# Performance work log

Measured on AMD Instinct MI355X. Metric: run time of the kernel, lower is better.

Reference implementation:

```python
import jax, jax.numpy as jnp
import numpy as np

B, T, IN, H, OUT = 32, 1024, 256, 768, 128


def setup_inputs() -> dict:
    key = jax.random.key(0)
    ks = jax.random.split(key, 11)
    s = 0.05
    return {
        "x": jax.random.normal(ks[0], (B, T, IN), dtype=jnp.float32),
        "W_ih0": jax.random.normal(ks[1], (4 * H, IN), dtype=jnp.float32) * s,
        "W_hh0": jax.random.normal(ks[2], (4 * H, H), dtype=jnp.float32) * s,
        "b_ih0": jax.random.normal(ks[3], (4 * H,), dtype=jnp.float32) * s,
        "b_hh0": jax.random.normal(ks[4], (4 * H,), dtype=jnp.float32) * s,
        "W_ih1": jax.random.normal(ks[5], (4 * H, H), dtype=jnp.float32) * s,
        "W_hh1": jax.random.normal(ks[6], (4 * H, H), dtype=jnp.float32) * s,
        "b_ih1": jax.random.normal(ks[7], (4 * H,), dtype=jnp.float32) * s,
        "b_hh1": jax.random.normal(ks[8], (4 * H,), dtype=jnp.float32) * s,
        "W_lin": jax.random.normal(ks[9], (OUT, H), dtype=jnp.float32) * s,
        "b_lin": jax.random.normal(ks[10], (OUT,), dtype=jnp.float32) * s,
    }


def _lstm_layer(x_btd, W_ih, W_hh, b_ih, b_hh):
    # Input-side GEMM for all timesteps at once: [B,T,4H]
    xg = jnp.einsum("btd,gd->btg", x_btd, W_ih) + b_ih + b_hh
    xg = jnp.swapaxes(xg, 0, 1)  # time-major [T,B,4H]
    h0 = jnp.zeros((x_btd.shape[0], W_hh.shape[1]), x_btd.dtype)

    def step(carry, gx):
        h, c = carry
        g = gx + h @ W_hh.T  # [B,4H]
        i, f, gg, o = jnp.split(g, 4, axis=-1)  # PyTorch gate order i,f,g,o
        i, f, o = jax.nn.sigmoid(i), jax.nn.sigmoid(f), jax.nn.sigmoid(o)
        c = f * c + i * jnp.tanh(gg)
        h = o * jnp.tanh(c)
        return (h, c), h

    _, hs = jax.lax.scan(step, (h0, h0), xg)  # hs: [T,B,H]
    return jnp.swapaxes(hs, 0, 1)  # [B,T,H]


def reference(x, W_ih0, W_hh0, b_ih0, b_hh0, W_ih1, W_hh1, b_ih1, b_hh1, W_lin, b_lin):
    h1 = _lstm_layer(x, W_ih0, W_hh0, b_ih0, b_hh0)
    h2 = _lstm_layer(h1, W_ih1, W_hh1, b_ih1, b_hh1)  # eval mode: inter-layer dropout off
    return jnp.einsum("bth,oh->bto", h2, W_lin) + b_lin
```

## Files before the change

### kernel.cpp

```cpp
#include <hip/hip_runtime.h>

#define Tt    1024
#define INF   256
#define Hh    768
#define OUTF  128

#define NWG_L0  48
#define NWG_L1  48
#define NWG_LIN 2
#define NWG     (NWG_L0 + NWG_L1 + NWG_LIN)
#define NTHR    1024

typedef unsigned int       u32;
typedef unsigned long long u64;
typedef unsigned short     u16;
typedef __attribute__((ext_vector_type(8))) short bf16x8;
typedef __attribute__((ext_vector_type(4))) float f32x4;

#define PROG_OFF 0
#define HA_OFF   16384
#define HB_OFF   (HA_OFF + 3*49152)
#define WS_BYTES (HB_OFF + 3*49152)
#define HPS      24576

#define ASTR_B 1552
#define RSLAB  272
#define RROW   17

__device__ __forceinline__ float sigf(float v){ return 1.0f/(1.0f+__expf(-v)); }
__device__ __forceinline__ float tanhfast(float x){
    const float cx = fminf(fmaxf(x, -15.f), 15.f);
    const float e  = __expf(2.f * cx);
    return (e - 1.f) / (e + 1.f);
}
__device__ __forceinline__ u16 f2bf(float f){
    u32 u = __float_as_uint(f);
    return (u16)((u + 0x7fffu + ((u>>16)&1u)) >> 16);
}
__device__ __forceinline__ void st32ws(u16* p, u32 v){
    __hip_atomic_store((u32*)p, v, __ATOMIC_RELAXED, __HIP_MEMORY_SCOPE_AGENT);
}
__device__ __forceinline__ u32 ldu32(const u32* p){
    return __hip_atomic_load(p, __ATOMIC_RELAXED, __HIP_MEMORY_SCOPE_AGENT);
}
__device__ __forceinline__ void stu32(u32* p, u32 v){
    __hip_atomic_store(p, v, __ATOMIC_RELAXED, __HIP_MEMORY_SCOPE_AGENT);
}
__device__ __forceinline__ void ld16x3(const u16* p0, const u16* p1, const u16* p2,
                                       f32x4& r0, f32x4& r1, f32x4& r2){
    asm volatile(
        "global_load_dwordx4 %0, %3, off sc0 sc1\n\t"
        "global_load_dwordx4 %1, %4, off sc0 sc1\n\t"
        "global_load_dwordx4 %2, %5, off sc0 sc1\n\t"
        "s_waitcnt vmcnt(0)"
        : "=&v"(r0), "=&v"(r1), "=&v"(r2)
        : "v"(p0), "v"(p1), "v"(p2)
        : "memory");
}
__device__ __forceinline__ void ld16x6(const u16* p0, const u16* p1, const u16* p2,
                                       const u16* p3, const u16* p4, const u16* p5,
                                       f32x4& r0, f32x4& r1, f32x4& r2,
                                       f32x4& r3, f32x4& r4, f32x4& r5){
    asm volatile(
        "global_load_dwordx4 %0, %6, off sc0 sc1\n\t"
        "global_load_dwordx4 %1, %7, off sc0 sc1\n\t"
        "global_load_dwordx4 %2, %8, off sc0 sc1\n\t"
        "global_load_dwordx4 %3, %9, off sc0 sc1\n\t"
        "global_load_dwordx4 %4, %10, off sc0 sc1\n\t"
        "global_load_dwordx4 %5, %11, off sc0 sc1\n\t"
        "s_waitcnt vmcnt(0)"
        : "=&v"(r0), "=&v"(r1), "=&v"(r2), "=&v"(r3), "=&v"(r4), "=&v"(r5)
        : "v"(p0), "v"(p1), "v"(p2), "v"(p3), "v"(p4), "v"(p5)
        : "memory");
}

__device__ __forceinline__ void waitlines(u32* prog, int base, int cnt, u32 thr, int lane){
    bool ok = (lane >= cnt);
    int guard = 0;
    while (guard < (1 << 24)) {
        if (!ok) ok = (ldu32(prog + (base + lane) * 32) >= thr);
        if (__ballot(ok) == ~0ull) break;
        __builtin_amdgcn_s_sleep(1);
        ++guard;
    }
}

__global__ void prologue(char* ws){
    int i = blockIdx.x * 256 + threadIdx.x;
    if (i < WS_BYTES / 4)
        __hip_atomic_store(((u32*)ws) + i, 0u, __ATOMIC_RELAXED, __HIP_MEMORY_SCOPE_AGENT);
}

__device__ __forceinline__ bf16x8 load8w(const float* p){
    float4 v0 = *(const float4*)(p);
    float4 v1 = *(const float4*)(p + 4);
    bf16x8 r;
    r[0]=(short)f2bf(v0.x); r[1]=(short)f2bf(v0.y); r[2]=(short)f2bf(v0.z); r[3]=(short)f2bf(v0.w);
    r[4]=(short)f2bf(v1.x); r[5]=(short)f2bf(v1.y); r[6]=(short)f2bf(v1.z); r[7]=(short)f2bf(v1.w);
    return r;
}

__global__ __launch_bounds__(NTHR) void lstm_persist(
    const float* __restrict__ x,
    const float* __restrict__ Wih0, const float* __restrict__ Whh0,
    const float* __restrict__ bih0, const float* __restrict__ bhh0,
    const float* __restrict__ Wih1, const float* __restrict__ Whh1,
    const float* __restrict__ bih1, const float* __restrict__ bhh1,
    const float* __restrict__ Wlin, const float* __restrict__ blin,
    float* __restrict__ out, char* ws)
{
    u32* prog = (u32*)(ws + PROG_OFF);
    u16* hA   = (u16*)(ws + HA_OFF);
    u16* hB   = (u16*)(ws + HB_OFF);

    const int wg  = blockIdx.x;
    const int tid = threadIdx.x;

    __shared__ __align__(16) char smem[49664];
    char*  actb = smem;
    float* red  = (float*)smem;

    const int lane = tid & 63, w = tid >> 6;
    const int quad = lane >> 4, nl = lane & 15;
    const int nt = w >> 2, ks = w & 3;
    const int b3 = tid >> 5, q = tid & 31;

    const int role  = (wg < NWG_L0) ? 0 : ((wg < NWG_L0 + NWG_L1) ? 1 : 2);
    const int jbase = (role == 0) ? wg * 16 : ((role == 1) ? (wg - NWG_L0) * 16 : 0);
    const int obase = (role == 2) ? (wg - NWG_L0 - NWG_L1) * 64 : 0;

    bf16x8 bfr[12];
    if (role == 0) {
        const int grow = nt * Hh + jbase + nl;
        #pragma unroll
        for (int fi = 0; fi < 8; ++fi) {
            const int c = fi >> 2, fc = fi & 3;
            const int ka = c * 512 + ks * 128 + fc * 32 + quad * 8;
            const float* p = (ka < 256) ? (Wih0 + (size_t)grow * 256 + ka)
                                        : (Whh0 + (size_t)grow * 768 + (ka - 256));
            bfr[fi] = load8w(p);
        }
    } else if (role == 1) {
        const int grow = nt * Hh + jbase + nl;
        #pragma unroll
        for (int fi = 0; fi < 12; ++fi) {
            const int c = fi / 6, fc = fi % 6;
            const int ka = c * 768 + ks * 192 + fc * 32 + quad * 8;
            const float* p = (ka < 768) ? (Wih1 + (size_t)grow * 768 + ka)
                                        : (Whh1 + (size_t)grow * 768 + (ka - 768));
            bfr[fi] = load8w(p);
        }
    } else {
        const int row = obase + nt * 16 + nl;
        #pragma unroll
        for (int fi = 0; fi < 6; ++fi) {
            const int ka = ks * 192 + fi * 32 + quad * 8;
            bfr[fi] = load8w(Wlin + (size_t)row * 768 + ka);
        }
    }

    float ba0=0,ba1=0,ba2=0,ba3=0, bb0=0,bb1=0,bb2=0,bb3=0, creg0=0, creg1=0;
    float bl0 = 0.f, bl1 = 0.f;
    if (role < 2 && tid < 256) {
        const int jg0 = jbase + 2 * (tid >> 5), jg1 = jg0 + 1;
        const float* bi = (role == 0) ? bih0 : bih1;
        const float* bh = (role == 0) ? bhh0 : bhh1;
        ba0 = bi[jg0]        + bh[jg0];        bb0 = bi[jg1]        + bh[jg1];
        ba1 = bi[768 + jg0]  + bh[768 + jg0];  bb1 = bi[768 + jg1]  + bh[768 + jg1];
        ba2 = bi[1536 + jg0] + bh[1536 + jg0]; bb2 = bi[1536 + jg1] + bh[1536 + jg1];
        ba3 = bi[2304 + jg0] + bh[2304 + jg0]; bb3 = bi[2304 + jg1] + bh[2304 + jg1];
    }
    if (role == 2) {
        bl0 = blin[obase + (tid >> 5)];
        bl1 = blin[obase + 32 + (tid >> 5)];
    }

    for (int s = 0; s < Tt + 2; ++s) {
        const bool active = (role == 0) ? (s < Tt)
                          : (role == 1) ? (s >= 1 && s <= Tt)
                          :               (s >= 2);
        const int par_wA = s % 3;
        const int par_rA = (s + 2) % 3;
        const int par_wB = (s + 2) % 3;
        const int par_rB = (s + 1) % 3;

        if (active && w == 0) {
            if (role == 0) {
                if (s >= 1) waitlines(prog, 0, 48, (u32)s, lane);
                if (s >= 2) waitlines(prog, 48, 48, (u32)(s - 1), lane);
            } else if (role == 1) {
                waitlines(prog, 48, 48, (u32)s, lane);
                {
                    const u32 thr2 = (lane < 48) ? (u32)s : (u32)(s - 1);
                    const int idx  = (lane < 48) ? lane : (96 + (lane - 48));
                    bool ok = (lane >= 50);
                    int guard = 0;
                    while (guard < (1 << 24)) {
                        if (!ok) ok = (ldu32(prog + idx * 32) >= thr2);
                        if (__ballot(ok) == ~0ull) break;
                        __builtin_amdgcn_s_sleep(1);
                        ++guard;
                    }
                }
            } else {
                waitlines(prog, 48, 48, (u32)s, lane);
            }
        }
        __syncthreads();

        if (active) {
            f32x4 acc0 = {0.f,0.f,0.f,0.f}, acc1 = {0.f,0.f,0.f,0.f};

            if (role == 0) {
                const float* xs = x + ((size_t)b3 * Tt + s) * INF + q * 8;
                const float4 v0 = *(const float4*)xs;
                const float4 v1 = *(const float4*)(xs + 4);
                const u16* hp = hA + (size_t)par_rA * HPS + b3 * 768;
                f32x4 h0, h1, h2;
                ld16x3(hp + q * 8, hp + 256 + q * 8, hp + 512 + q * 8, h0, h1, h2);
                {
                    uint4 xv;
                    xv.x = (u32)f2bf(v0.x) | ((u32)f2bf(v0.y) << 16);
                    xv.y = (u32)f2bf(v0.z) | ((u32)f2bf(v0.w) << 16);
                    xv.z = (u32)f2bf(v1.x) | ((u32)f2bf(v1.y) << 16);
                    xv.w = (u32)f2bf(v1.z) | ((u32)f2bf(v1.w) << 16);
                    *(uint4*)(actb + b3 * ASTR_B + q * 16) = xv;
                    *(f32x4*)(actb + b3 * ASTR_B + 512 + q * 16) = h0;
                }
                __syncthreads();
                #pragma unroll
                for (int fc = 0; fc < 4; ++fc) {
                    const int koff = ks * 128 + fc * 32 + quad * 8;
                    bf16x8 a0 = *(const bf16x8*)(actb + nl * ASTR_B + koff * 2);
                    bf16x8 a1 = *(const bf16x8*)(actb + (16 + nl) * ASTR_B + koff * 2);
                    acc0 = __builtin_amdgcn_mfma_f32_16x16x32_bf16(a0, bfr[fc], acc0, 0, 0, 0);
                    acc1 = __builtin_amdgcn_mfma_f32_16x16x32_bf16(a1, bfr[fc], acc1, 0, 0, 0);
                }
                __syncthreads();
                *(f32x4*)(actb + b3 * ASTR_B + q * 16)       = h1;
                *(f32x4*)(actb + b3 * ASTR_B + 512 + q * 16) = h2;
                __syncthreads();
                #pragma unroll
                for (int fc = 0; fc < 4; ++fc) {
                    const int koff = ks * 128 + fc * 32 + quad * 8;
                    bf16x8 a0 = *(const bf16x8*)(actb + nl * ASTR_B + koff * 2);
                    bf16x8 a1 = *(const bf16x8*)(actb + (16 + nl) * ASTR_B + koff * 2);
                    acc0 = __builtin_amdgcn_mfma_f32_16x16x32_bf16(a0, bfr[4 + fc], acc0, 0, 0, 0);
                    acc1 = __builtin_amdgcn_mfma_f32_16x16x32_bf16(a1, bfr[4 + fc], acc1, 0, 0, 0);
                }
                __syncthreads();
            } else if (role == 1) {
                const u16* pA = hA + (size_t)par_rA * HPS + b3 * 768;
                const u16* pB = hB + (size_t)par_rB * HPS + b3 * 768;
                f32x4 a0, a1, a2, bq0, bq1, bq2;
                ld16x6(pA + q * 8, pA + 256 + q * 8, pA + 512 + q * 8,
                       pB + q * 8, pB + 256 + q * 8, pB + 512 + q * 8,
                       a0, a1, a2, bq0, bq1, bq2);
                *(f32x4*)(actb + b3 * ASTR_B + q * 16)        = a0;
                *(f32x4*)(actb + b3 * ASTR_B + 512 + q * 16)  = a1;
                *(f32x4*)(actb + b3 * ASTR_B + 1024 + q * 16) = a2;
                __syncthreads();
                #pragma unroll
                for (int fc = 0; fc < 6; ++fc) {
                    const int koff = ks * 192 + fc * 32 + quad * 8;
                    bf16x8 f0 = *(const bf16x8*)(actb + nl * ASTR_B + koff * 2);
                    bf16x8 f1 = *(const bf16x8*)(actb + (16 + nl) * ASTR_B + koff * 2);
                    acc0 = __builtin_amdgcn_mfma_f32_16x16x32_bf16(f0, bfr[fc], acc0, 0, 0, 0);
                    acc1 = __builtin_amdgcn_mfma_f32_16x16x32_bf16(f1, bfr[fc], acc1, 0, 0, 0);
                }
                __syncthreads();
                *(f32x4*)(actb + b3 * ASTR_B + q * 16)        = bq0;
                *(f32x4*)(actb + b3 * ASTR_B + 512 + q * 16)  = bq1;
                *(f32x4*)(actb + b3 * ASTR_B + 1024 + q * 16) = bq2;
                __syncthreads();
                #pragma unroll
                for (int fc = 0; fc < 6; ++fc) {
                    const int koff = ks * 192 + fc * 32 + quad * 8;
                    bf16x8 f0 = *(const bf16x8*)(actb + nl * ASTR_B + koff * 2);
                    bf16x8 f1 = *(const bf16x8*)(actb + (16 + nl) * ASTR_B + koff * 2);
                    acc0 = __builtin_amdgcn_mfma_f32_16x16x32_bf16(f0, bfr[6 + fc], acc0, 0, 0, 0);
                    acc1 = __builtin_amdgcn_mfma_f32_16x16x32_bf16(f1, bfr[6 + fc], acc1, 0, 0, 0);
                }
                __syncthreads();
            } else {
                const u16* pB = hB + (size_t)par_rB * HPS + b3 * 768;
                f32x4 bq0, bq1, bq2;
                ld16x3(pB + q * 8, pB + 256 + q * 8, pB + 512 + q * 8, bq0, bq1, bq2);
                *(f32x4*)(actb + b3 * ASTR_B + q * 16)        = bq0;
                *(f32x4*)(actb + b3 * ASTR_B + 512 + q * 16)  = bq1;
                *(f32x4*)(actb + b3 * ASTR_B + 1024 + q * 16) = bq2;
                __syncthreads();
                #pragma unroll
                for (int fc = 0; fc < 6; ++fc) {
                    const int koff = ks * 192 + fc * 32 + quad * 8;
                    bf16x8 f0 = *(const bf16x8*)(actb + nl * ASTR_B + koff * 2);
                    bf16x8 f1 = *(const bf16x8*)(actb + (16 + nl) * ASTR_B + koff * 2);
                    acc0 = __builtin_amdgcn_mfma_f32_16x16x32_bf16(f0, bfr[fc], acc0, 0, 0, 0);
                    acc1 = __builtin_amdgcn_mfma_f32_16x16x32_bf16(f1, bfr[fc], acc1, 0, 0, 0);
                }
                __syncthreads();
            }

            *(f32x4*)(red + (size_t)((nt * 2 + 0) * 4 + ks) * RSLAB + nl * RROW + quad * 4) = acc0;
            *(f32x4*)(red + (size_t)((nt * 2 + 1) * 4 + ks) * RSLAB + nl * RROW + quad * 4) = acc1;
            __syncthreads();

            if (role == 2) {
                const int r2 = tid >> 5, bb = tid & 31;
                const int mtr = bb >> 4, mr = bb & 15;
                const int nt0 = r2 >> 4, nr0 = r2 & 15;
                const int nt1 = (r2 + 32) >> 4, nr1 = (r2 + 32) & 15;
                float s0 = 0.f, s1 = 0.f;
                #pragma unroll
                for (int k2 = 0; k2 < 4; ++k2) {
                    s0 += red[(size_t)((nt0 * 2 + mtr) * 4 + k2) * RSLAB + nr0 * RROW + mr];
                    s1 += red[(size_t)((nt1 * 2 + mtr) * 4 + k2) * RSLAB + nr1 * RROW + mr];
                }
                const int v = s - 2;
                float* o = out + ((size_t)bb * Tt + v) * OUTF + obase;
                o[r2]      = s0 + bl0;
                o[32 + r2] = s1 + bl1;
            } else if (tid < 256) {
                const int jj = tid >> 5, b2 = tid & 31;
                const int mt = b2 >> 4, mr = b2 & 15;
                const int j0 = 2 * jj, j1 = 2 * jj + 1;
                float p0a=0,p1a=0,p2a=0,p3a=0, p0b=0,p1b=0,p2b=0,p3b=0;
                #pragma unroll
                for (int k2 = 0; k2 < 4; ++k2) {
                    p0a += red[(size_t)((0 * 2 + mt) * 4 + k2) * RSLAB + j0 * RROW + mr];
                    p1a += red[(size_t)((1 * 2 + mt) * 4 + k2) * RSLAB + j0 * RROW + mr];
                    p2a += red[(size_t)((2 * 2 + mt) * 4 + k2) * RSLAB + j0 * RROW + mr];
                    p3a += red[(size_t)((3 * 2 + mt) * 4 + k2) * RSLAB + j0 * RROW + mr];
                    p0b += red[(size_t)((0 * 2 + mt) * 4 + k2) * RSLAB + j1 * RROW + mr];
                    p1b += red[(size_t)((1 * 2 + mt) * 4 + k2) * RSLAB + j1 * RROW + mr];
                    p2b += red[(size_t)((2 * 2 + mt) * 4 + k2) * RSLAB + j1 * RROW + mr];
                    p3b += red[(size_t)((3 * 2 + mt) * 4 + k2) * RSLAB + j1 * RROW + mr];
                }
                const float ig0 = sigf(ba0 + p0a), fg0 = sigf(ba1 + p1a);
                const float gv0 = tanhfast(ba2 + p2a), og0 = sigf(ba3 + p3a);
                creg0 = fg0 * creg0 + ig0 * gv0;
                const float h0 = og0 * tanhfast(creg0);
                const float ig1 = sigf(bb0 + p0b), fg1 = sigf(bb1 + p1b);
                const float gv1 = tanhfast(bb2 + p2b), og1 = sigf(bb3 + p3b);
                creg1 = fg1 * creg1 + ig1 * gv1;
                const float h1 = og1 * tanhfast(creg1);
                u16* dst = (role == 0) ? (hA + (size_t)par_wA * HPS)
                                       : (hB + (size_t)par_wB * HPS);
                st32ws(dst + b2 * 768 + jbase + j0, (u32)f2bf(h0) | ((u32)f2bf(h1) << 16));
            }
        }

        __syncthreads();
        if (tid == 0) stu32(prog + wg * 32, (u32)(s + 1));
    }
}

extern "C" void kernel_launch(void* const* d_in, const int* in_sizes, int n_in,
                              void* d_out, int out_size, void* d_ws, size_t ws_size,
                              hipStream_t stream)
{
    const float* x    = (const float*)d_in[0];
    const float* Wih0 = (const float*)d_in[1];
    const float* Whh0 = (const float*)d_in[2];
    const float* bih0 = (const float*)d_in[3];
    const float* bhh0 = (const float*)d_in[4];
    const float* Wih1 = (const float*)d_in[5];
    const float* Whh1 = (const float*)d_in[6];
    const float* bih1 = (const float*)d_in[7];
    const float* bhh1 = (const float*)d_in[8];
    const float* Wlin = (const float*)d_in[9];
    const float* blin = (const float*)d_in[10];
    float* out = (float*)d_out;
    char*  ws  = (char*)d_ws;

    hipLaunchKernelGGL(prologue, dim3(304), dim3(256), 0, stream, ws);
    hipLaunchKernelGGL(lstm_persist, dim3(NWG), dim3(NTHR), 0, stream,
                       x, Wih0, Whh0, bih0, bhh0,
                       Wih1, Whh1, bih1, bhh1,
                       Wlin, blin, out, ws);
}
```

Measured before the change: 6.240 ms.

## Split LSTM layers across more workgroups with counter barriers and direct register activation loads

Doubles the workgroups per LSTM layer, giving each 8 hidden units instead of 16, and gives each wave a 16-row batch slice across 8 K-splits. Per-workgroup progress flags polled with ballot are replaced by shared atomic counters in rotating slots, and a workgroup-local ready flag lets the input-side waves start before the recurrent dependency is satisfied. Activations are loaded straight from global memory into MFMA operand registers rather than staged through shared memory, which removes several __syncthreads per step. In exchange there are more workgroups contending on atomics, more reduction partials, and redundant global loads of activations per wave.

```diff
diff --git a/kernel.cpp b/kernel.cpp
--- a/kernel.cpp
+++ b/kernel.cpp
@@ -5,27 +5,26 @@
 #define Hh    768
 #define OUTF  128
 
-#define NWG_L0  48
-#define NWG_L1  48
+#define NWG_L0  96
+#define NWG_L1  96
 #define NWG_LIN 2
 #define NWG     (NWG_L0 + NWG_L1 + NWG_LIN)
 #define NTHR    1024
+#define NIT     (Tt + 2)
 
 typedef unsigned int       u32;
-typedef unsigned long long u64;
 typedef unsigned short     u16;
 typedef __attribute__((ext_vector_type(8))) short bf16x8;
 typedef __attribute__((ext_vector_type(4))) float f32x4;
 
-#define PROG_OFF 0
+#define CTR_OFF  0
+#define HPS      24576
 #define HA_OFF   16384
-#define HB_OFF   (HA_OFF + 3*49152)
-#define WS_BYTES (HB_OFF + 3*49152)
-#define HPS      24576
-
-#define ASTR_B 1552
-#define RSLAB  272
-#define RROW   17
+#define HB_OFF   (HA_OFF + 3 * 49152)
+#define WS_BYTES (HB_OFF + 3 * 49152)
+
+#define RSLAB 272
+#define RROW  17
 
 __device__ __forceinline__ float sigf(float v){ return 1.0f/(1.0f+__expf(-v)); }
 __device__ __forceinline__ float tanhfast(float x){
@@ -43,45 +42,51 @@
 __device__ __forceinline__ u32 ldu32(const u32* p){
     return __hip_atomic_load(p, __ATOMIC_RELAXED, __HIP_MEMORY_SCOPE_AGENT);
 }
-__device__ __forceinline__ void stu32(u32* p, u32 v){
-    __hip_atomic_store(p, v, __ATOMIC_RELAXED, __HIP_MEMORY_SCOPE_AGENT);
-}
-__device__ __forceinline__ void ld16x3(const u16* p0, const u16* p1, const u16* p2,
-                                       f32x4& r0, f32x4& r1, f32x4& r2){
+
+__device__ __forceinline__ void issue4w(const u16* p, f32x4& r0, f32x4& r1,
+                                        f32x4& r2, f32x4& r3){
     asm volatile(
-        "global_load_dwordx4 %0, %3, off sc0 sc1\n\t"
-        "global_load_dwordx4 %1, %4, off sc0 sc1\n\t"
-        "global_load_dwordx4 %2, %5, off sc0 sc1\n\t"
+        "global_load_dwordx4 %0, %4, off sc0 sc1\n\t"
+        "global_load_dwordx4 %1, %4, off offset:64 sc0 sc1\n\t"
+        "global_load_dwordx4 %2, %4, off offset:128 sc0 sc1\n\t"
+        "global_load_dwordx4 %3, %4, off offset:192 sc0 sc1\n\t"
         "s_waitcnt vmcnt(0)"
-        : "=&v"(r0), "=&v"(r1), "=&v"(r2)
-        : "v"(p0), "v"(p1), "v"(p2)
-        : "memory");
-}
-__device__ __forceinline__ void ld16x6(const u16* p0, const u16* p1, const u16* p2,
-                                       const u16* p3, const u16* p4, const u16* p5,
-                                       f32x4& r0, f32x4& r1, f32x4& r2,
-                                       f32x4& r3, f32x4& r4, f32x4& r5){
+        : "=&v"(r0), "=&v"(r1), "=&v"(r2), "=&v"(r3)
+        : "v"(p) : "memory");
+}
+__device__ __forceinline__ void issue6w(const u16* p, f32x4& r0, f32x4& r1,
+                                        f32x4& r2, f32x4& r3, f32x4& r4, f32x4& r5){
     asm volatile(
         "global_load_dwordx4 %0, %6, off sc0 sc1\n\t"
-        "global_load_dwordx4 %1, %7, off sc0 sc1\n\t"
-        "global_load_dwordx4 %2, %8, off sc0 sc1\n\t"
-        "global_load_dwordx4 %3, %9, off sc0 sc1\n\t"
-        "global_load_dwordx4 %4, %10, off sc0 sc1\n\t"
-        "global_load_dwordx4 %5, %11, off sc0 sc1\n\t"
+        "global_load_dwordx4 %1, %6, off offset:64 sc0 sc1\n\t"
+        "global_load_dwordx4 %2, %6, off offset:128 sc0 sc1\n\t"
+        "global_load_dwordx4 %3, %6, off offset:192 sc0 sc1\n\t"
+        "global_load_dwordx4 %4, %6, off offset:256 sc0 sc1\n\t"
+        "global_load_dwordx4 %5, %6, off offset:320 sc0 sc1\n\t"
         "s_waitcnt vmcnt(0)"
         : "=&v"(r0), "=&v"(r1), "=&v"(r2), "=&v"(r3), "=&v"(r4), "=&v"(r5)
-        : "v"(p0), "v"(p1), "v"(p2), "v"(p3), "v"(p4), "v"(p5)
-        : "memory");
-}
-
-__device__ __forceinline__ void waitlines(u32* prog, int base, int cnt, u32 thr, int lane){
-    bool ok = (lane >= cnt);
-    int guard = 0;
-    while (guard < (1 << 24)) {
-        if (!ok) ok = (ldu32(prog + (base + lane) * 32) >= thr);
-        if (__ballot(ok) == ~0ull) break;
-        __builtin_amdgcn_s_sleep(1);
-        ++guard;
+        : "v"(p) : "memory");
+}
+
+#define BC(v) __builtin_bit_cast(bf16x8, v)
+
+__device__ __forceinline__ void wait1p(const u32* a, u32 ta){
+    int g = 0;
+    while (g < (1 << 24) && ldu32(a) < ta) { __builtin_amdgcn_s_sleep(1); ++g; }
+}
+__device__ __forceinline__ void wait2p(const u32* a, u32 ta, const u32* b, u32 tb){
+    int g = 0;
+    while (g < (1 << 24)) {
+        if (ldu32(a) >= ta && ldu32(b) >= tb) break;
+        __builtin_amdgcn_s_sleep(1); ++g;
+    }
+}
+__device__ __forceinline__ void wait3p(const u32* a, u32 ta, const u32* b, u32 tb,
+                                       const u32* c, u32 tc){
+    int g = 0;
+    while (g < (1 << 24)) {
+        if (ldu32(a) >= ta && ldu32(b) >= tb && ldu32(c) >= tc) break;
+        __builtin_amdgcn_s_sleep(1); ++g;
     }
 }
 
@@ -109,59 +114,62 @@
     const float* __restrict__ Wlin, const float* __restrict__ blin,
     float* __restrict__ out, char* ws)
 {
-    u32* prog = (u32*)(ws + PROG_OFF);
-    u16* hA   = (u16*)(ws + HA_OFF);
-    u16* hB   = (u16*)(ws + HB_OFF);
+    u32* ctr = (u32*)(ws + CTR_OFF);
+    u16* hA  = (u16*)(ws + HA_OFF);
+    u16* hB  = (u16*)(ws + HB_OFF);
 
     const int wg  = blockIdx.x;
     const int tid = threadIdx.x;
 
-    __shared__ __align__(16) char smem[49664];
-    char*  actb = smem;
-    float* red  = (float*)smem;
+    __shared__ __align__(16) float red[32 * RSLAB];
+    __shared__ u32 rdy;
 
     const int lane = tid & 63, w = tid >> 6;
     const int quad = lane >> 4, nl = lane & 15;
-    const int nt = w >> 2, ks = w & 3;
-    const int b3 = tid >> 5, q = tid & 31;
+    const int mwv = w >> 3, ks = w & 7;
+    const int ntL = w >> 2, ksL = w & 3;
 
     const int role  = (wg < NWG_L0) ? 0 : ((wg < NWG_L0 + NWG_L1) ? 1 : 2);
-    const int jbase = (role == 0) ? wg * 16 : ((role == 1) ? (wg - NWG_L0) * 16 : 0);
+    const int jbase = (role == 0) ? wg * 8 : ((role == 1) ? (wg - NWG_L0) * 8 : 0);
     const int obase = (role == 2) ? (wg - NWG_L0 - NWG_L1) * 64 : 0;
 
     bf16x8 bfr[12];
     if (role == 0) {
-        const int grow = nt * Hh + jbase + nl;
         #pragma unroll
-        for (int fi = 0; fi < 8; ++fi) {
-            const int c = fi >> 2, fc = fi & 3;
-            const int ka = c * 512 + ks * 128 + fc * 32 + quad * 8;
-            const float* p = (ka < 256) ? (Wih0 + (size_t)grow * 256 + ka)
-                                        : (Whh0 + (size_t)grow * 768 + (ka - 256));
-            bfr[fi] = load8w(p);
+        for (int nt = 0; nt < 2; ++nt) {
+            const int grow = (nt * 2 + (nl >> 3)) * Hh + jbase + (nl & 7);
+            #pragma unroll
+            for (int fi = 0; fi < 4; ++fi) {
+                const int ka = ks * 128 + fi * 32 + quad * 8;
+                const float* p = (ka < 256) ? (Wih0 + (size_t)grow * 256 + ka)
+                                            : (Whh0 + (size_t)grow * 768 + (ka - 256));
+                bfr[nt * 4 + fi] = load8w(p);
+            }
         }
     } else if (role == 1) {
-        const int grow = nt * Hh + jbase + nl;
         #pragma unroll
-        for (int fi = 0; fi < 12; ++fi) {
-            const int c = fi / 6, fc = fi % 6;
-            const int ka = c * 768 + ks * 192 + fc * 32 + quad * 8;
-            const float* p = (ka < 768) ? (Wih1 + (size_t)grow * 768 + ka)
-                                        : (Whh1 + (size_t)grow * 768 + (ka - 768));
-            bfr[fi] = load8w(p);
+        for (int nt = 0; nt < 2; ++nt) {
+            const int grow = (nt * 2 + (nl >> 3)) * Hh + jbase + (nl & 7);
+            #pragma unroll
+            for (int fi = 0; fi < 6; ++fi) {
+                const int ka = ks * 192 + fi * 32 + quad * 8;
+                const float* p = (ka < 768) ? (Wih1 + (size_t)grow * 768 + ka)
+                                            : (Whh1 + (size_t)grow * 768 + (ka - 768));
+                bfr[nt * 6 + fi] = load8w(p);
+            }
         }
     } else {
-        const int row = obase + nt * 16 + nl;
+        const int row = obase + ntL * 16 + nl;
         #pragma unroll
         for (int fi = 0; fi < 6; ++fi) {
-            const int ka = ks * 192 + fi * 32 + quad * 8;
+            const int ka = ksL * 192 + fi * 32 + quad * 8;
             bfr[fi] = load8w(Wlin + (size_t)row * 768 + ka);
         }
     }
 
     float ba0=0,ba1=0,ba2=0,ba3=0, bb0=0,bb1=0,bb2=0,bb3=0, creg0=0, creg1=0;
     float bl0 = 0.f, bl1 = 0.f;
-    if (role < 2 && tid < 256) {
+    if (role < 2 && tid < 128) {
         const int jg0 = jbase + 2 * (tid >> 5), jg1 = jg0 + 1;
         const float* bi = (role == 0) ? bih0 : bih1;
         const float* bh = (role == 0) ? bhh0 : bhh1;
@@ -175,183 +183,169 @@
         bl1 = blin[obase + 32 + (tid >> 5)];
     }
 
-    for (int s = 0; s < Tt + 2; ++s) {
-        const bool active = (role == 0) ? (s < Tt)
-                          : (role == 1) ? (s >= 1 && s <= Tt)
-                          :               (s >= 2);
+    if (tid == 0) __hip_atomic_store(&rdy, 0u, __ATOMIC_RELAXED, __HIP_MEMORY_SCOPE_WORKGROUP);
+    __syncthreads();
+
+    for (int s = 0; s < NIT; ++s) {
         const int par_wA = s % 3;
         const int par_rA = (s + 2) % 3;
         const int par_wB = (s + 2) % 3;
         const int par_rB = (s + 1) % 3;
+        const bool active = (role == 0) ? (s < Tt)
+                          : (role == 1) ? (s >= 1 && s <= Tt)
+                          :               (s >= 2);
 
         if (active && w == 0) {
             if (role == 0) {
-                if (s >= 1) waitlines(prog, 0, 48, (u32)s, lane);
-                if (s >= 2) waitlines(prog, 48, 48, (u32)(s - 1), lane);
+                if (s >= 2)
+                    wait2p(ctr + (0*4 + ((s-1)&3))*32, 96u*((u32)(s-1)/4u + 1u),
+                           ctr + (1*4 + ((s-2)&3))*32, 96u*((u32)(s-2)/4u + 1u));
+                else if (s == 1)
+                    wait1p(ctr + (0*4 + 0)*32, 96u);
             } else if (role == 1) {
-                waitlines(prog, 48, 48, (u32)s, lane);
-                {
-                    const u32 thr2 = (lane < 48) ? (u32)s : (u32)(s - 1);
-                    const int idx  = (lane < 48) ? lane : (96 + (lane - 48));
-                    bool ok = (lane >= 50);
-                    int guard = 0;
-                    while (guard < (1 << 24)) {
-                        if (!ok) ok = (ldu32(prog + idx * 32) >= thr2);
-                        if (__ballot(ok) == ~0ull) break;
-                        __builtin_amdgcn_s_sleep(1);
-                        ++guard;
-                    }
-                }
+                if (s >= 2)
+                    wait3p(ctr + (0*4 + ((s-1)&3))*32, 96u*((u32)(s-1)/4u + 1u),
+                           ctr + (1*4 + ((s-1)&3))*32, 96u*((u32)(s-1)/4u + 1u),
+                           ctr + (2*4 + ((s-2)&3))*32,  2u*((u32)(s-2)/4u + 1u));
+                else
+                    wait2p(ctr + (0*4 + 0)*32, 96u, ctr + (1*4 + 0)*32, 96u);
             } else {
-                waitlines(prog, 48, 48, (u32)s, lane);
-            }
-        }
-        __syncthreads();
+                wait1p(ctr + (1*4 + ((s-1)&3))*32, 96u*((u32)(s-1)/4u + 1u));
+            }
+            if (lane == 0)
+                __hip_atomic_store(&rdy, (u32)(s + 1), __ATOMIC_RELAXED, __HIP_MEMORY_SCOPE_WORKGROUP);
+        }
+        if (active && w != 0 && (role != 0 || ks >= 2)) {
+            int g = 0;
+            while (g < (1 << 24) &&
+                   __hip_atomic_load(&rdy, __ATOMIC_RELAXED, __HIP_MEMORY_SCOPE_WORKGROUP) < (u32)(s + 1)) {
+                __builtin_amdgcn_s_sleep(1); ++g;
+            }
+        }
 
         if (active) {
             f32x4 acc0 = {0.f,0.f,0.f,0.f}, acc1 = {0.f,0.f,0.f,0.f};
 
             if (role == 0) {
-                const float* xs = x + ((size_t)b3 * Tt + s) * INF + q * 8;
-                const float4 v0 = *(const float4*)xs;
-                const float4 v1 = *(const float4*)(xs + 4);
-                const u16* hp = hA + (size_t)par_rA * HPS + b3 * 768;
-                f32x4 h0, h1, h2;
-                ld16x3(hp + q * 8, hp + 256 + q * 8, hp + 512 + q * 8, h0, h1, h2);
-                {
-                    uint4 xv;
-                    xv.x = (u32)f2bf(v0.x) | ((u32)f2bf(v0.y) << 16);
-                    xv.y = (u32)f2bf(v0.z) | ((u32)f2bf(v0.w) << 16);
-                    xv.z = (u32)f2bf(v1.x) | ((u32)f2bf(v1.y) << 16);
-                    xv.w = (u32)f2bf(v1.z) | ((u32)f2bf(v1.w) << 16);
-                    *(uint4*)(actb + b3 * ASTR_B + q * 16) = xv;
-                    *(f32x4*)(actb + b3 * ASTR_B + 512 + q * 16) = h0;
+                if (ks < 2) {
+                    const float* xr = x + ((size_t)(mwv*16 + nl) * Tt + s) * INF
+                                        + ks * 128 + quad * 8;
+                    #pragma unroll
+                    for (int fi = 0; fi < 4; ++fi) {
+                        const bf16x8 af = load8w(xr + fi * 32);
+                        acc0 = __builtin_amdgcn_mfma_f32_16x16x32_bf16(af, bfr[fi],     acc0, 0,0,0);
+                        acc1 = __builtin_amdgcn_mfma_f32_16x16x32_bf16(af, bfr[4 + fi], acc1, 0,0,0);
+                    }
+                } else {
+                    const u16* pm = hA + (size_t)par_rA * HPS + (size_t)(mwv*16 + nl) * 768
+                                       + (ks - 2) * 128 + quad * 8;
+                    f32x4 q0, q1, q2, q3;
+                    issue4w(pm, q0, q1, q2, q3);
+                    acc0 = __builtin_amdgcn_mfma_f32_16x16x32_bf16(BC(q0), bfr[0], acc0, 0,0,0);
+                    acc1 = __builtin_amdgcn_mfma_f32_16x16x32_bf16(BC(q0), bfr[4], acc1, 0,0,0);
+                    acc0 = __builtin_amdgcn_mfma_f32_16x16x32_bf16(BC(q1), bfr[1], acc0, 0,0,0);
+                    acc1 = __builtin_amdgcn_mfma_f32_16x16x32_bf16(BC(q1), bfr[5], acc1, 0,0,0);
+                    acc0 = __builtin_amdgcn_mfma_f32_16x16x32_bf16(BC(q2), bfr[2], acc0, 0,0,0);
+                    acc1 = __builtin_amdgcn_mfma_f32_16x16x32_bf16(BC(q2), bfr[6], acc1, 0,0,0);
+                    acc0 = __builtin_amdgcn_mfma_f32_16x16x32_bf16(BC(q3), bfr[3], acc0, 0,0,0);
+                    acc1 = __builtin_amdgcn_mfma_f32_16x16x32_bf16(BC(q3), bfr[7], acc1, 0,0,0);
                 }
-                __syncthreads();
-                #pragma unroll
-                for (int fc = 0; fc < 4; ++fc) {
-                    const int koff = ks * 128 + fc * 32 + quad * 8;
-                    bf16x8 a0 = *(const bf16x8*)(actb + nl * ASTR_B + koff * 2);
-                    bf16x8 a1 = *(const bf16x8*)(actb + (16 + nl) * ASTR_B + koff * 2);
-                    acc0 = __builtin_amdgcn_mfma_f32_16x16x32_bf16(a0, bfr[fc], acc0, 0, 0, 0);
-                    acc1 = __builtin_amdgcn_mfma_f32_16x16x32_bf16(a1, bfr[fc], acc1, 0, 0, 0);
-                }
-                __syncthreads();
-                *(f32x4*)(actb + b3 * ASTR_B + q * 16)       = h1;
-                *(f32x4*)(actb + b3 * ASTR_B + 512 + q * 16) = h2;
-                __syncthreads();
-                #pragma unroll
-                for (int fc = 0; fc < 4; ++fc) {
-                    const int koff = ks * 128 + fc * 32 + quad * 8;
-                    bf16x8 a0 = *(const bf16x8*)(actb + nl * ASTR_B + koff * 2);
-                    bf16x8 a1 = *(const bf16x8*)(actb + (16 + nl) * ASTR_B + koff * 2);
-                    acc0 = __builtin_amdgcn_mfma_f32_16x16x32_bf16(a0, bfr[4 + fc], acc0, 0, 0, 0);
-                    acc1 = __builtin_amdgcn_mfma_f32_16x16x32_bf16(a1, bfr[4 + fc], acc1, 0, 0, 0);
-                }
-                __syncthreads();
             } else if (role == 1) {
-                const u16* pA = hA + (size_t)par_rA * HPS + b3 * 768;
-                const u16* pB = hB + (size_t)par_rB * HPS + b3 * 768;
-                f32x4 a0, a1, a2, bq0, bq1, bq2;
-                ld16x6(pA + q * 8, pA + 256 + q * 8, pA + 512 + q * 8,
-                       pB + q * 8, pB + 256 + q * 8, pB + 512 + q * 8,
-                       a0, a1, a2, bq0, bq1, bq2);
-                *(f32x4*)(actb + b3 * ASTR_B + q * 16)        = a0;
-                *(f32x4*)(actb + b3 * ASTR_B + 512 + q * 16)  = a1;
-                *(f32x4*)(actb + b3 * ASTR_B + 1024 + q * 16) = a2;
-                __syncthreads();
-                #pragma unroll
-                for (int fc = 0; fc < 6; ++fc) {
-                    const int koff = ks * 192 + fc * 32 + quad * 8;
-                    bf16x8 f0 = *(const bf16x8*)(actb + nl * ASTR_B + koff * 2);
-                    bf16x8 f1 = *(const bf16x8*)(actb + (16 + nl) * ASTR_B + koff * 2);
-                    acc0 = __builtin_amdgcn_mfma_f32_16x16x32_bf16(f0, bfr[fc], acc0, 0, 0, 0);
-                    acc1 = __builtin_amdgcn_mfma_f32_16x16x32_bf16(f1, bfr[fc], acc1, 0, 0, 0);
-                }
-                __syncthreads();
-                *(f32x4*)(actb + b3 * ASTR_B + q * 16)        = bq0;
-                *(f32x4*)(actb + b3 * ASTR_B + 512 + q * 16)  = bq1;
-                *(f32x4*)(actb + b3 * ASTR_B + 1024 + q * 16) = bq2;
-                __syncthreads();
-                #pragma unroll
-                for (int fc = 0; fc < 6; ++fc) {
-                    const int koff = ks * 192 + fc * 32 + quad * 8;
-                    bf16x8 f0 = *(const bf16x8*)(actb + nl * ASTR_B + koff * 2);
-                    bf16x8 f1 = *(const bf16x8*)(actb + (16 + nl) * ASTR_B + koff * 2);
-                    acc0 = __builtin_amdgcn_mfma_f32_16x16x32_bf16(f0, bfr[6 + fc], acc0, 0, 0, 0);
-                    acc1 = __builtin_amdgcn_mfma_f32_16x16x32_bf16(f1, bfr[6 + fc], acc1, 0, 0, 0);
-                }
-                __syncthreads();
+                const u16* base = (ks < 4) ? (hA + (size_t)par_rA * HPS)
+                                           : (hB + (size_t)par_rB * HPS);
+                const u16* pm = base + (size_t)(mwv*16 + nl) * 768 + (ks & 3) * 192 + quad * 8;
+                f32x4 q0, q1, q2, q3, q4, q5;
+                issue6w(pm, q0, q1, q2, q3, q4, q5);
+                acc0 = __builtin_amdgcn_mfma_f32_16x16x32_bf16(BC(q0), bfr[0],  acc0, 0,0,0);
+                acc1 = __builtin_amdgcn_mfma_f32_16x16x32_bf16(BC(q0), bfr[6],  acc1, 0,0,0);
+                acc0 = __builtin_amdgcn_mfma_f32_16x16x32_bf16(BC(q1), bfr[1],  acc0, 0,0,0);
+                acc1 = __builtin_amdgcn_mfma_f32_16x16x32_bf16(BC(q1), bfr[7],  acc1, 0,0,0);
+                acc0 = __builtin_amdgcn_mfma_f32_16x16x32_bf16(BC(q2), bfr[2],  acc0, 0,0,0);
+                acc1 = __builtin_amdgcn_mfma_f32_16x16x32_bf16(BC(q2), bfr[8],  acc1, 0,0,0);
+                acc0 = __builtin_amdgcn_mfma_f32_16x16x32_bf16(BC(q3), bfr[3],  acc0, 0,0,0);
+                acc1 = __builtin_amdgcn_mfma_f32_16x16x32_bf16(BC(q3), bfr[9],  acc1, 0,0,0);
+                acc0 = __builtin_amdgcn_mfma_f32_16x16x32_bf16(BC(q4), bfr[4],  acc0, 0,0,0);
+                acc1 = __builtin_amdgcn_mfma_f32_16x16x32_bf16(BC(q4), bfr[10], acc1, 0,0,0);
+                acc0 = __builtin_amdgcn_mfma_f32_16x16x32_bf16(BC(q5), bfr[5],  acc0, 0,0,0);
+                acc1 = __builtin_amdgcn_mfma_f32_16x16x32_bf16(BC(q5), bfr[11], acc1, 0,0,0);
             } else {
-                const u16* pB = hB + (size_t)par_rB * HPS + b3 * 768;
-                f32x4 bq0, bq1, bq2;
-                ld16x3(pB + q * 8, pB + 256 + q * 8, pB + 512 + q * 8, bq0, bq1, bq2);
-                *(f32x4*)(actb + b3 * ASTR_B + q * 16)        = bq0;
-                *(f32x4*)(actb + b3 * ASTR_B + 512 + q * 16)  = bq1;
-                *(f32x4*)(actb + b3 * ASTR_B + 1024 + q * 16) = bq2;
-                __syncthreads();
-                #pragma unroll
-                for (int fc = 0; fc < 6; ++fc) {
-                    const int koff = ks * 192 + fc * 32 + quad * 8;
-                    bf16x8 f0 = *(const bf16x8*)(actb + nl * ASTR_B + koff * 2);
-                    bf16x8 f1 = *(const bf16x8*)(actb + (16 + nl) * ASTR_B + koff * 2);
-                    acc0 = __builtin_amdgcn_mfma_f32_16x16x32_bf16(f0, bfr[fc], acc0, 0, 0, 0);
-                    acc1 = __builtin_amdgcn_mfma_f32_16x16x32_bf16(f1, bfr[fc], acc1, 0, 0, 0);
-                }
-                __syncthreads();
-            }
-
-            *(f32x4*)(red + (size_t)((nt * 2 + 0) * 4 + ks) * RSLAB + nl * RROW + quad * 4) = acc0;
-            *(f32x4*)(red + (size_t)((nt * 2 + 1) * 4 + ks) * RSLAB + nl * RROW + quad * 4) = acc1;
+                const u16* pb = hB + (size_t)par_rB * HPS + (size_t)nl * 768 + ksL * 192 + quad * 8;
+                f32x4 q0, q1, q2, q3, q4, q5;
+                issue6w(pb, q0, q1, q2, q3, q4, q5);
+                acc0 = __builtin_amdgcn_mfma_f32_16x16x32_bf16(BC(q0), bfr[0], acc0, 0,0,0);
+                acc0 = __builtin_amdgcn_mfma_f32_16x16x32_bf16(BC(q1), bfr[1], acc0, 0,0,0);
+                acc0 = __builtin_amdgcn_mfma_f32_16x16x32_bf16(BC(q2), bfr[2], acc0, 0,0,0);
+                acc0 = __builtin_amdgcn_mfma_f32_16x16x32_bf16(BC(q3), bfr[3], acc0, 0,0,0);
+                acc0 = __builtin_amdgcn_mfma_f32_16x16x32_bf16(BC(q4), bfr[4], acc0, 0,0,0);
+                acc0 = __builtin_amdgcn_mfma_f32_16x16x32_bf16(BC(q5), bfr[5], acc0, 0,0,0);
+                issue6w(pb + 16 * 768, q0, q1, q2, q3, q4, q5);
+                acc1 = __builtin_amdgcn_mfma_f32_16x16x32_bf16(BC(q0), bfr[0], acc1, 0,0,0);
+                acc1 = __builtin_amdgcn_mfma_f32_16x16x32_bf16(BC(q1), bfr[1], acc1, 0,0,0);
+                acc1 = __builtin_amdgcn_mfma_f32_16x16x32_bf16(BC(q2), bfr[2], acc1, 0,0,0);
+                acc1 = __builtin_amdgcn_mfma_f32_16x16x32_bf16(BC(q3), bfr[3], acc1, 0,0,0);
+                acc1 = __builtin_amdgcn_mfma_f32_16x16x32_bf16(BC(q4), bfr[4], acc1, 0,0,0);
+                acc1 = __builtin_amdgcn_mfma_f32_16x16x32_bf16(BC(q5), bfr[5], acc1, 0,0,0);
+            }
+
+            if (role < 2) {
+                *(f32x4*)&red[(size_t)((mwv    ) * 8 + ks) * RSLAB + nl * RROW + quad * 4] = acc0;
+                *(f32x4*)&red[(size_t)((2 + mwv) * 8 + ks) * RSLAB + nl * RROW + quad * 4] = acc1;
+            } else {
+                *(f32x4*)&red[(size_t)((ntL * 2 + 0) * 4 + ksL) * RSLAB + nl * RROW + quad * 4] = acc0;
+                *(f32x4*)&red[(size_t)((ntL * 2 + 1) * 4 + ksL) * RSLAB + nl * RROW + quad * 4] = acc1;
+            }
             __syncthreads();
 
             if (role == 2) {
+                const int v = s - 2;
                 const int r2 = tid >> 5, bb = tid & 31;
-                const int mtr = bb >> 4, mr = bb & 15;
+                const int mtr = bb >> 4, mr2 = bb & 15;
                 const int nt0 = r2 >> 4, nr0 = r2 & 15;
                 const int nt1 = (r2 + 32) >> 4, nr1 = (r2 + 32) & 15;
                 float s0 = 0.f, s1 = 0.f;
                 #pragma unroll
                 for (int k2 = 0; k2 < 4; ++k2) {
-                    s0 += red[(size_t)((nt0 * 2 + mtr) * 4 + k2) * RSLAB + nr0 * RROW + mr];
-                    s1 += red[(size_t)((nt1 * 2 + mtr) * 4 + k2) * RSLAB + nr1 * RROW + mr];
+                    s0 += red[(size_t)((nt0 * 2 + mtr) * 4 + k2) * RSLAB + nr0 * RROW + mr2];
+                    s1 += red[(size_t)((nt1 * 2 + mtr) * 4 + k2) * RSLAB + nr1 * RROW + mr2];
                 }
-                const int v = s - 2;
                 float* o = out + ((size_t)bb * Tt + v) * OUTF + obase;
                 o[r2]      = s0 + bl0;
                 o[32 + r2] = s1 + bl1;
-            } else if (tid < 256) {
+            } else if (tid < 128) {
                 const int jj = tid >> 5, b2 = tid & 31;
                 const int mt = b2 >> 4, mr = b2 & 15;
-                const int j0 = 2 * jj, j1 = 2 * jj + 1;
-                float p0a=0,p1a=0,p2a=0,p3a=0, p0b=0,p1b=0,p2b=0,p3b=0;
+                float pa[4], pb_[4];
                 #pragma unroll
-                for (int k2 = 0; k2 < 4; ++k2) {
-                    p0a += red[(size_t)((0 * 2 + mt) * 4 + k2) * RSLAB + j0 * RROW + mr];
-                    p1a += red[(size_t)((1 * 2 + mt) * 4 + k2) * RSLAB + j0 * RROW + mr];
-                    p2a += red[(size_t)((2 * 2 + mt) * 4 + k2) * RSLAB + j0 * RROW + mr];
-                    p3a += red[(size_t)((3 * 2 + mt) * 4 + k2) * RSLAB + j0 * RROW + mr];
-                    p0b += red[(size_t)((0 * 2 + mt) * 4 + k2) * RSLAB + j1 * RROW + mr];
-                    p1b += red[(size_t)((1 * 2 + mt) * 4 + k2) * RSLAB + j1 * RROW + mr];
-                    p2b += red[(size_t)((2 * 2 + mt) * 4 + k2) * RSLAB + j1 * RROW + mr];
-                    p3b += red[(size_t)((3 * 2 + mt) * 4 + k2) * RSLAB + j1 * RROW + mr];
+                for (int g = 0; g < 4; ++g) {
+                    const int sb = ((g >> 1) * 2 + mt) * 8;
+                    const int c0 = (g & 1) * 8 + 2 * jj;
+                    float s0 = 0.f, s1 = 0.f;
+                    #pragma unroll
+                    for (int k2 = 0; k2 < 8; ++k2) {
+                        s0 += red[(size_t)(sb + k2) * RSLAB + c0 * RROW + mr];
+                        s1 += red[(size_t)(sb + k2) * RSLAB + (c0 + 1) * RROW + mr];
+                    }
+                    pa[g] = s0; pb_[g] = s1;
                 }
-                const float ig0 = sigf(ba0 + p0a), fg0 = sigf(ba1 + p1a);
-                const float gv0 = tanhfast(ba2 + p2a), og0 = sigf(ba3 + p3a);
+                const float ig0 = sigf(ba0 + pa[0]), fg0 = sigf(ba1 + pa[1]);
+                const float gv0 = tanhfast(ba2 + pa[2]), og0 = sigf(ba3 + pa[3]);
                 creg0 = fg0 * creg0 + ig0 * gv0;
                 const float h0 = og0 * tanhfast(creg0);
-                const float ig1 = sigf(bb0 + p0b), fg1 = sigf(bb1 + p1b);
-                const float gv1 = tanhfast(bb2 + p2b), og1 = sigf(bb3 + p3b);
+                const float ig1 = sigf(bb0 + pb_[0]), fg1 = sigf(bb1 + pb_[1]);
+                const float gv1 = tanhfast(bb2 + pb_[2]), og1 = sigf(bb3 + pb_[3]);
                 creg1 = fg1 * creg1 + ig1 * gv1;
                 const float h1 = og1 * tanhfast(creg1);
                 u16* dst = (role == 0) ? (hA + (size_t)par_wA * HPS)
                                        : (hB + (size_t)par_wB * HPS);
-                st32ws(dst + b2 * 768 + jbase + j0, (u32)f2bf(h0) | ((u32)f2bf(h1) << 16));
+                st32ws(dst + b2 * 768 + jbase + 2 * jj,
+                       (u32)f2bf(h0) | ((u32)f2bf(h1) << 16));
             }
         }
 
         __syncthreads();
-        if (tid == 0) stu32(prog + wg * 32, (u32)(s + 1));
+        if (tid == 0)
+            __hip_atomic_fetch_add(ctr + ((size_t)(role * 4 + (s & 3))) * 32, 1u,
+                                   __ATOMIC_RELAXED, __HIP_MEMORY_SCOPE_AGENT);
     }
 }
 
```

Result: slower. 9.841 ms (+57.7%).
